# Kernel optimization log

Hardware: AMD Instinct MI355X
Metric: run time of the kernel (lower is better)

## Reference

```python
import jax, jax.numpy as jnp
import numpy as np

EPS = 1e-12  # torch F.normalize clamps the norm at 1e-12

def _l2norm(v, axis):
    n = jnp.sqrt(jnp.sum(v * v, axis=axis, keepdims=True))
    return v / jnp.maximum(n, EPS)

def setup_inputs() -> dict:
    key = jax.random.key(0)
    k1, k2, k3, k4 = jax.random.split(key, 4)
    N, C, H, W, K = 64, 64, 64, 64, 128
    alpha = 1.0
    x = jax.random.normal(k1, (N, C, H, W), dtype=jnp.float32)
    centroids = jax.random.uniform(k2, (K, C), dtype=jnp.float32)
    # conv is initialized from centroids (2*alpha*c, -alpha*||c||) but is an
    # independent parameter after init; keep the init relationship for realism.
    conv_w = 2.0 * alpha * centroids
    conv_b = -alpha * jnp.sqrt(jnp.sum(centroids * centroids, axis=1))
    return {"x": x, "centroids": centroids, "conv_w": conv_w, "conv_b": conv_b}

def reference(x, centroids, conv_w, conv_b):
    N, C, H, W = x.shape
    K = centroids.shape[0]
    # L2-normalize descriptors along channel dim
    xn = _l2norm(x, axis=1)                                   # [N,C,H,W]
    # 1x1 conv == per-pixel linear map C->K
    logits = jnp.einsum('nchw,kc->nkhw', xn, conv_w) + conv_b[None, :, None, None]
    sa = jax.nn.softmax(logits.reshape(N, K, H * W), axis=1)  # [N,K,HW]
    xf = xn.reshape(N, C, H * W)                              # [N,C,HW]
    # vlad[n,k,c] = sum_l sa[n,k,l] * (xf[n,c,l] - centroids[k,c])
    #            = (sa @ xf^T)[n,k,c] - sum_l sa[n,k,l] * centroids[k,c]
    vlad = jnp.einsum('nkl,ncl->nkc', sa, xf) - sa.sum(axis=-1)[:, :, None] * centroids[None]
    vlad = _l2norm(vlad, axis=2)            # intra-normalization per cluster
    vlad = vlad.reshape(N, K * C)
    vlad = _l2norm(vlad, axis=1)            # global L2 normalization
    return vlad
```

## Files before the change

kernel.cpp:

```cpp
#include <hip/hip_runtime.h>
#include <math.h>

#define NIMG   64
#define CDIM   64
#define HWPX   4096
#define KCL    128
#define TL     64
#define SHIFT  10.0f
#define RSQRT128 0.08838834764831845f

#define XP_S 72
#define XC_S 72
#define PH_S 72

typedef __attribute__((ext_vector_type(8))) short short8;
typedef __attribute__((ext_vector_type(4))) float f32x4;

#define MFMA(a, b, c) __builtin_amdgcn_mfma_f32_16x16x32_bf16((a), (b), (c), 0, 0, 0)

#define PERM_HI16 0x07060302u

#define BAR() do {                                          \
    asm volatile("s_waitcnt lgkmcnt(0)" ::: "memory");      \
    __builtin_amdgcn_s_barrier();                           \
    __builtin_amdgcn_sched_barrier(0);                      \
} while (0)

template <int NP>
__global__ __launch_bounds__(256, 2)
void netvlad_main(const float* __restrict__ x,
                  const float* __restrict__ conv_w,
                  const float* __restrict__ conv_b,
                  float* __restrict__ vout,
                  float* __restrict__ asout,
                  int use_atomic)
{
    constexpr int PIXPART = HWPX / NP;
    constexpr int NCHUNK  = PIXPART / TL;

    __shared__ __align__(16) short xp_hi[2][TL * XP_S], xp_lo[2][TL * XP_S];
    __shared__ __align__(16) short xc[2][CDIM * XC_S];
    __shared__ __align__(16) short ph[KCL * PH_S];
    __shared__ __align__(8) float2 redA2[2][4 * 32];
    __shared__ __align__(8) float2 sumP2[4 * 32];

    const int t   = threadIdx.x;
    const int w   = t >> 6;
    const int l   = t & 63;
    const int l15 = l & 15, l4 = l >> 4;
    const int n    = blockIdx.x / NP;
    const int part = blockIdx.x - n * NP;
    const int q    = t & 31;
    const int sg   = t >> 5;
    const int p0   = (q & 15) + ((q & 16) << 1);
    const int xslot = ((q >> 4) << 5) + 2 * (q & 15);

    short8 wh[2][2], wl[2][2];
    #pragma unroll
    for (int kt = 0; kt < 2; ++kt) {
        const int krow = (2 * w + kt) * 16 + l15;
        #pragma unroll
        for (int ks = 0; ks < 2; ++ks) {
            const float4* wp = (const float4*)(conv_w + krow * CDIM + ks * 32 + l4 * 8);
            float4 wa = wp[0], wb = wp[1];
            float wv[8] = {wa.x, wa.y, wa.z, wa.w, wb.x, wb.y, wb.z, wb.w};
            #pragma unroll
            for (int j = 0; j < 8; ++j) {
                unsigned u = __builtin_bit_cast(unsigned, wv[j]);
                wh[kt][ks][j] = (short)(u >> 16);
                float hf = __builtin_bit_cast(float, u & 0xffff0000u);
                wl[kt][ks][j] = (short)(__builtin_bit_cast(unsigned, wv[j] - hf) >> 16);
            }
        }
    }
    float cbr[2][4];
    #pragma unroll
    for (int kt = 0; kt < 2; ++kt)
        #pragma unroll
        for (int i = 0; i < 4; ++i)
            cbr[kt][i] = conv_b[(2 * w + kt) * 16 + l4 * 4 + i] - SHIFT;

    f32x4 acc2[2][4];
    #pragma unroll
    for (int a = 0; a < 2; ++a)
        #pragma unroll
        for (int b = 0; b < 4; ++b) acc2[a][b] = (f32x4)0.0f;
    float asr[2][4];
    #pragma unroll
    for (int a = 0; a < 2; ++a)
        #pragma unroll
        for (int i = 0; i < 4; ++i) asr[a][i] = 0.f;

    const float* xbase = x + (size_t)n * CDIM * HWPX + part * PIXPART;

    float xv0[8], xv1[8];

    #define LOADX(OFF) do {                                                 \
        _Pragma("unroll")                                                   \
        for (int j = 0; j < 8; ++j) {                                       \
            xv0[j] = xbase[(sg * 8 + j) * HWPX + (OFF) + p0];               \
            xv1[j] = xbase[(sg * 8 + j) * HWPX + (OFF) + p0 + 16];          \
        }                                                                   \
    } while (0)

    auto stage = [&](int buf) {
        float ssq0 = 0.f, ssq1 = 0.f;
        #pragma unroll
        for (int j = 0; j < 8; ++j) {
            ssq0 += xv0[j] * xv0[j];
            ssq1 += xv1[j] * xv1[j];
        }
        ssq0 += __shfl_xor(ssq0, 32);
        ssq1 += __shfl_xor(ssq1, 32);
        if (l < 32) redA2[buf][w * 32 + q] = make_float2(ssq0, ssq1);

        {
            unsigned uh[4], ul[4];
            #pragma unroll
            for (int jp = 0; jp < 4; ++jp) {
                const unsigned u0 = __builtin_bit_cast(unsigned, xv0[2 * jp]);
                const unsigned u1 = __builtin_bit_cast(unsigned, xv0[2 * jp + 1]);
                uh[jp] = __builtin_amdgcn_perm(u1, u0, PERM_HI16);
                const float h0 = __builtin_bit_cast(float, u0 & 0xffff0000u);
                const float h1 = __builtin_bit_cast(float, u1 & 0xffff0000u);
                const unsigned lo0 = __builtin_bit_cast(unsigned, xv0[2 * jp] - h0);
                const unsigned lo1 = __builtin_bit_cast(unsigned, xv0[2 * jp + 1] - h1);
                ul[jp] = __builtin_amdgcn_perm(lo1, lo0, PERM_HI16);
            }
            *(uint4*)&xp_hi[buf][p0 * XP_S + sg * 8] = make_uint4(uh[0], uh[1], uh[2], uh[3]);
            *(uint4*)&xp_lo[buf][p0 * XP_S + sg * 8] = make_uint4(ul[0], ul[1], ul[2], ul[3]);
        }
        {
            unsigned uh[4], ul[4];
            #pragma unroll
            for (int jp = 0; jp < 4; ++jp) {
                const unsigned u0 = __builtin_bit_cast(unsigned, xv1[2 * jp]);
                const unsigned u1 = __builtin_bit_cast(unsigned, xv1[2 * jp + 1]);
                uh[jp] = __builtin_amdgcn_perm(u1, u0, PERM_HI16);
                const float h0 = __builtin_bit_cast(float, u0 & 0xffff0000u);
                const float h1 = __builtin_bit_cast(float, u1 & 0xffff0000u);
                const unsigned lo0 = __builtin_bit_cast(unsigned, xv1[2 * jp] - h0);
                const unsigned lo1 = __builtin_bit_cast(unsigned, xv1[2 * jp + 1] - h1);
                ul[jp] = __builtin_amdgcn_perm(lo1, lo0, PERM_HI16);
            }
            *(uint4*)&xp_hi[buf][(p0 + 16) * XP_S + sg * 8] = make_uint4(uh[0], uh[1], uh[2], uh[3]);
            *(uint4*)&xp_lo[buf][(p0 + 16) * XP_S + sg * 8] = make_uint4(ul[0], ul[1], ul[2], ul[3]);
        }

        #pragma unroll
        for (int j = 0; j < 8; ++j) {
            unsigned pk;
            asm("v_cvt_pk_bf16_f32 %0, %1, %2"
                : "=v"(pk) : "v"(xv0[j]), "v"(xv1[j]));
            *(unsigned*)&xc[buf][(sg * 8 + j) * XC_S + xslot] = pk;
        }
    };

    LOADX(0);
    stage(0);
    if (NCHUNK > 1) LOADX(TL);
    BAR();

    for (int ch = 0; ch < NCHUNK; ++ch) {
        const int cur = ch & 1;

        if (ch + 1 < NCHUNK) {
            stage(cur ^ 1);
            if (ch + 2 < NCHUNK) LOADX((ch + 2) * TL);
        }

        f32x4 a1[2][4];
        #pragma unroll
        for (int a = 0; a < 2; ++a)
            #pragma unroll
            for (int b = 0; b < 4; ++b) a1[a][b] = (f32x4)0.0f;
        #pragma unroll
        for (int ks = 0; ks < 2; ++ks) {
            #pragma unroll
            for (int pt = 0; pt < 4; ++pt) {
                short8 bh = *(short8*)&xp_hi[cur][(pt * 16 + l15) * XP_S + ks * 32 + l4 * 8];
                short8 bl = *(short8*)&xp_lo[cur][(pt * 16 + l15) * XP_S + ks * 32 + l4 * 8];
                #pragma unroll
                for (int kt = 0; kt < 2; ++kt) {
                    a1[kt][pt] = MFMA(wh[kt][ks], bh, a1[kt][pt]);
                    a1[kt][pt] = MFMA(wh[kt][ks], bl, a1[kt][pt]);
                    a1[kt][pt] = MFMA(wl[kt][ks], bh, a1[kt][pt]);
                }
            }
        }

        float2 ra0 = redA2[cur][l15],           ra1 = redA2[cur][32 + l15];
        float2 ra2 = redA2[cur][64 + l15],      ra3 = redA2[cur][96 + l15];
        float2 rb0 = redA2[cur][16 + l15],      rb1 = redA2[cur][48 + l15];
        float2 rb2 = redA2[cur][80 + l15],      rb3 = redA2[cur][112 + l15];
        float rn[4];
        rn[0] = 1.0f / fmaxf(sqrtf((ra0.x + ra1.x) + (ra2.x + ra3.x)), 1e-12f);
        rn[1] = 1.0f / fmaxf(sqrtf((ra0.y + ra1.y) + (ra2.y + ra3.y)), 1e-12f);
        rn[2] = 1.0f / fmaxf(sqrtf((rb0.x + rb1.x) + (rb2.x + rb3.x)), 1e-12f);
        rn[3] = 1.0f / fmaxf(sqrtf((rb0.y + rb1.y) + (rb2.y + rb3.y)), 1e-12f);

        float e[2][4][4], sp[4] = {0.f, 0.f, 0.f, 0.f};
        #pragma unroll
        for (int kt = 0; kt < 2; ++kt)
            #pragma unroll
            for (int pt = 0; pt < 4; ++pt)
                #pragma unroll
                for (int i = 0; i < 4; ++i) {
                    float ev = __expf(fmaf(a1[kt][pt][i], rn[pt], cbr[kt][i]));
                    e[kt][pt][i] = ev;
                    sp[pt] += ev;
                }
        #pragma unroll
        for (int pt = 0; pt < 4; ++pt) {
            sp[pt] += __shfl_xor(sp[pt], 16);
            sp[pt] += __shfl_xor(sp[pt], 32);
        }
        if (l4 == 0)      sumP2[w * 32 + l15]      = make_float2(sp[0], sp[1]);
        else if (l4 == 1) sumP2[w * 32 + 16 + l15] = make_float2(sp[2], sp[3]);
        BAR();

        float2 q0 = sumP2[l15],       q1 = sumP2[32 + l15];
        float2 q2 = sumP2[64 + l15],  q3 = sumP2[96 + l15];
        float2 r0 = sumP2[16 + l15],  r1 = sumP2[48 + l15];
        float2 r2 = sumP2[80 + l15],  r3 = sumP2[112 + l15];
        float rden[4], rdn2[4];
        rden[0] = 1.0f / ((q0.x + q1.x) + (q2.x + q3.x));
        rden[1] = 1.0f / ((q0.y + q1.y) + (q2.y + q3.y));
        rden[2] = 1.0f / ((r0.x + r1.x) + (r2.x + r3.x));
        rden[3] = 1.0f / ((r0.y + r1.y) + (r2.y + r3.y));
        #pragma unroll
        for (int pt = 0; pt < 4; ++pt) rdn2[pt] = rden[pt] * rn[pt];

        #pragma unroll
        for (int kt = 0; kt < 2; ++kt)
            #pragma unroll
            for (int i = 0; i < 4; ++i) {
                const int row = (2 * w + kt) * 16 + l4 * 4 + i;
                const float e0 = e[kt][0][i], e1 = e[kt][1][i];
                const float e2 = e[kt][2][i], e3 = e[kt][3][i];
                asr[kt][i] = fmaf(e0, rden[0], asr[kt][i]);
                asr[kt][i] = fmaf(e1, rden[1], asr[kt][i]);
                asr[kt][i] = fmaf(e2, rden[2], asr[kt][i]);
                asr[kt][i] = fmaf(e3, rden[3], asr[kt][i]);
                const float p0f = e0 * rdn2[0], p1f = e1 * rdn2[1];
                const float p2f = e2 * rdn2[2], p3f = e3 * rdn2[3];
                unsigned pk01, pk23;
                asm("v_cvt_pk_bf16_f32 %0, %1, %2" : "=v"(pk01) : "v"(p0f), "v"(p1f));
                asm("v_cvt_pk_bf16_f32 %0, %1, %2" : "=v"(pk23) : "v"(p2f), "v"(p3f));
                *(unsigned*)&ph[row * PH_S + 2 * l15]      = pk01;
                *(unsigned*)&ph[row * PH_S + 32 + 2 * l15] = pk23;
            }

        {
            short8 xh2[4][2];
            #pragma unroll
            for (int ct = 0; ct < 4; ++ct)
                #pragma unroll
                for (int h = 0; h < 2; ++h)
                    xh2[ct][h] = *(short8*)&xc[cur][(ct * 16 + l15) * XC_S + h * 32 + l4 * 8];
            #pragma unroll
            for (int kt = 0; kt < 2; ++kt) {
                short8 ah0 = *(short8*)&ph[((2 * w + kt) * 16 + l15) * PH_S + l4 * 8];
                short8 ah1 = *(short8*)&ph[((2 * w + kt) * 16 + l15) * PH_S + 32 + l4 * 8];
                #pragma unroll
                for (int ct = 0; ct < 4; ++ct) {
                    acc2[kt][ct] = MFMA(ah0, xh2[ct][0], acc2[kt][ct]);
                    acc2[kt][ct] = MFMA(ah1, xh2[ct][1], acc2[kt][ct]);
                }
            }
        }
        BAR();
    }
    #undef LOADX

    float* vg = use_atomic ? vout + (size_t)n * KCL * CDIM
                           : vout + (size_t)blockIdx.x * KCL * CDIM;
    #pragma unroll
    for (int kt = 0; kt < 2; ++kt)
        #pragma unroll
        for (int ct = 0; ct < 4; ++ct)
            #pragma unroll
            for (int i = 0; i < 4; ++i) {
                const int row = (2 * w + kt) * 16 + l4 * 4 + i;
                const int col = ct * 16 + l15;
                if (use_atomic) atomicAdd(&vg[row * CDIM + col], acc2[kt][ct][i]);
                else            vg[row * CDIM + col] = acc2[kt][ct][i];
            }

    #pragma unroll
    for (int kt = 0; kt < 2; ++kt)
        #pragma unroll
        for (int i = 0; i < 4; ++i) {
            float v = asr[kt][i];
            v += __shfl_xor(v, 1); v += __shfl_xor(v, 2);
            v += __shfl_xor(v, 4); v += __shfl_xor(v, 8);
            if (l15 == 0) {
                const int row = (2 * w + kt) * 16 + l4 * 4 + i;
                if (use_atomic) atomicAdd(&asout[n * KCL + row], v);
                else            asout[blockIdx.x * KCL + row] = v;
            }
        }
}

template <int NPARTS>
__global__ __launch_bounds__(256)
void netvlad_finalize(const float* __restrict__ vpart,
                      const float* __restrict__ aspart,
                      const float* __restrict__ cent,
                      float* __restrict__ out)
{
    const int t = threadIdx.x;
    const int n  = blockIdx.x >> 3;
    const int kg = blockIdx.x & 7;
    const int k  = kg * 16 + (t >> 4);
    const int c0 = (t & 15) * 4;

    float vsum[4] = {0.f, 0.f, 0.f, 0.f};
    float av = 0.f;
    #pragma unroll
    for (int pt = 0; pt < NPARTS; ++pt) {
        const float* vg = vpart + (((size_t)n * NPARTS + pt) * KCL + k) * CDIM + c0;
        float4 a = *(const float4*)vg;
        vsum[0] += a.x; vsum[1] += a.y; vsum[2] += a.z; vsum[3] += a.w;
        av += aspart[(n * NPARTS + pt) * KCL + k];
    }

    float4 cq = *(const float4*)(cent + k * CDIM + c0);
    float cc[4] = {cq.x, cq.y, cq.z, cq.w};
    float ss = 0.f;
    #pragma unroll
    for (int j = 0; j < 4; ++j) {
        vsum[j] -= av * cc[j];
        ss += vsum[j] * vsum[j];
    }
    ss += __shfl_xor(ss, 1); ss += __shfl_xor(ss, 2);
    ss += __shfl_xor(ss, 4); ss += __shfl_xor(ss, 8);
    const float s = (1.0f / fmaxf(sqrtf(ss), 1e-12f)) * RSQRT128;

    float4 o;
    o.x = vsum[0] * s; o.y = vsum[1] * s; o.z = vsum[2] * s; o.w = vsum[3] * s;
    *(float4*)(out + (size_t)n * KCL * CDIM + k * CDIM + c0) = o;
}

extern "C" void kernel_launch(void* const* d_in, const int* in_sizes, int n_in,
                              void* d_out, int out_size, void* d_ws, size_t ws_size,
                              hipStream_t stream) {
    const float* x     = (const float*)d_in[0];
    const float* cent  = (const float*)d_in[1];
    const float* convw = (const float*)d_in[2];
    const float* convb = (const float*)d_in[3];
    float* out = (float*)d_out;

    const size_t need8 = (size_t)NIMG * 8 * (KCL * CDIM + KCL) * sizeof(float);

    if (ws_size >= need8) {
        float* vws  = (float*)d_ws;
        float* asws = vws + (size_t)NIMG * 8 * KCL * CDIM;
        netvlad_main<8><<<dim3(NIMG * 8), dim3(256), 0, stream>>>(
            x, convw, convb, vws, asws, 0);
        netvlad_finalize<8><<<dim3(NIMG * 8), dim3(256), 0, stream>>>(
            vws, asws, cent, out);
    } else {
        float* vws  = (float*)d_ws;
        float* asws = vws + (size_t)NIMG * KCL * CDIM;
        const size_t zb = (size_t)NIMG * (KCL * CDIM + KCL) * sizeof(float);
        hipMemsetAsync(d_ws, 0, zb, stream);
        netvlad_main<8><<<dim3(NIMG * 8), dim3(256), 0, stream>>>(
            x, convw, convb, vws, asws, 1);
        netvlad_finalize<1><<<dim3(NIMG * 8), dim3(256), 0, stream>>>(
            vws, asws, cent, out);
    }
}
```

Before: 122.1 us.

## Split waves 2x2 over clusters and pixels to cut cross-wave softmax reduction

Reassigns the four waves from each owning 32 clusters across all 64 pixels to a 2x2 split: each wave owns 64 clusters and 32 pixels of a chunk. The softmax denominator now needs only one partner wave's partial sum instead of four, and each wave loads fewer pixel B-fragments while reusing more weight fragments per load. In exchange, register use for weights, accumulators and softmax values doubles, which is a concern under launch_bounds(256,2). The two pixel halves' VLAD accumulators also need an extra LDS reduction and barrier at the end, and half the waves sit idle during the output writes.

Result: slower. 126.9 us (+3.9%).

```diff
diff --git a/kernel.cpp b/kernel.cpp
--- a/kernel.cpp
+++ b/kernel.cpp
@@ -42,12 +42,14 @@
     __shared__ __align__(16) short xc[2][CDIM * XC_S];
     __shared__ __align__(16) short ph[KCL * PH_S];
     __shared__ __align__(8) float2 redA2[2][4 * 32];
-    __shared__ __align__(8) float2 sumP2[4 * 32];
+    __shared__ __align__(8) float2 sumP2[4 * 16];
 
     const int t   = threadIdx.x;
     const int w   = t >> 6;
     const int l   = t & 63;
     const int l15 = l & 15, l4 = l >> 4;
+    const int kh  = w & 1;
+    const int h   = w >> 1;
     const int n    = blockIdx.x / NP;
     const int part = blockIdx.x - n * NP;
     const int q    = t & 31;
@@ -55,10 +57,10 @@
     const int p0   = (q & 15) + ((q & 16) << 1);
     const int xslot = ((q >> 4) << 5) + 2 * (q & 15);
 
-    short8 wh[2][2], wl[2][2];
-    #pragma unroll
-    for (int kt = 0; kt < 2; ++kt) {
-        const int krow = (2 * w + kt) * 16 + l15;
+    short8 wh[4][2], wl[4][2];
+    #pragma unroll
+    for (int kt = 0; kt < 4; ++kt) {
+        const int krow = kh * 64 + kt * 16 + l15;
         #pragma unroll
         for (int ks = 0; ks < 2; ++ks) {
             const float4* wp = (const float4*)(conv_w + krow * CDIM + ks * 32 + l4 * 8);
@@ -73,21 +75,21 @@
             }
         }
     }
-    float cbr[2][4];
-    #pragma unroll
-    for (int kt = 0; kt < 2; ++kt)
+    float cbr[4][4];
+    #pragma unroll
+    for (int kt = 0; kt < 4; ++kt)
         #pragma unroll
         for (int i = 0; i < 4; ++i)
-            cbr[kt][i] = conv_b[(2 * w + kt) * 16 + l4 * 4 + i] - SHIFT;
-
-    f32x4 acc2[2][4];
-    #pragma unroll
-    for (int a = 0; a < 2; ++a)
+            cbr[kt][i] = conv_b[kh * 64 + kt * 16 + l4 * 4 + i] - SHIFT;
+
+    f32x4 acc2[4][4];
+    #pragma unroll
+    for (int a = 0; a < 4; ++a)
         #pragma unroll
         for (int b = 0; b < 4; ++b) acc2[a][b] = (f32x4)0.0f;
-    float asr[2][4];
-    #pragma unroll
-    for (int a = 0; a < 2; ++a)
+    float asr[4][4];
+    #pragma unroll
+    for (int a = 0; a < 4; ++a)
         #pragma unroll
         for (int i = 0; i < 4; ++i) asr[a][i] = 0.f;
 
@@ -169,19 +171,20 @@
             if (ch + 2 < NCHUNK) LOADX((ch + 2) * TL);
         }
 
-        f32x4 a1[2][4];
-        #pragma unroll
-        for (int a = 0; a < 2; ++a)
-            #pragma unroll
-            for (int b = 0; b < 4; ++b) a1[a][b] = (f32x4)0.0f;
+        f32x4 a1[4][2];
+        #pragma unroll
+        for (int a = 0; a < 4; ++a)
+            #pragma unroll
+            for (int b = 0; b < 2; ++b) a1[a][b] = (f32x4)0.0f;
         #pragma unroll
         for (int ks = 0; ks < 2; ++ks) {
             #pragma unroll
-            for (int pt = 0; pt < 4; ++pt) {
-                short8 bh = *(short8*)&xp_hi[cur][(pt * 16 + l15) * XP_S + ks * 32 + l4 * 8];
-                short8 bl = *(short8*)&xp_lo[cur][(pt * 16 + l15) * XP_S + ks * 32 + l4 * 8];
+            for (int pt = 0; pt < 2; ++pt) {
+                const int prow = h * 32 + pt * 16 + l15;
+                short8 bh = *(short8*)&xp_hi[cur][prow * XP_S + ks * 32 + l4 * 8];
+                short8 bl = *(short8*)&xp_lo[cur][prow * XP_S + ks * 32 + l4 * 8];
                 #pragma unroll
-                for (int kt = 0; kt < 2; ++kt) {
+                for (int kt = 0; kt < 4; ++kt) {
                     a1[kt][pt] = MFMA(wh[kt][ks], bh, a1[kt][pt]);
                     a1[kt][pt] = MFMA(wh[kt][ks], bl, a1[kt][pt]);
                     a1[kt][pt] = MFMA(wl[kt][ks], bh, a1[kt][pt]);
@@ -189,21 +192,18 @@
             }
         }
 
-        float2 ra0 = redA2[cur][l15],           ra1 = redA2[cur][32 + l15];
-        float2 ra2 = redA2[cur][64 + l15],      ra3 = redA2[cur][96 + l15];
-        float2 rb0 = redA2[cur][16 + l15],      rb1 = redA2[cur][48 + l15];
-        float2 rb2 = redA2[cur][80 + l15],      rb3 = redA2[cur][112 + l15];
-        float rn[4];
+        const int qi = h * 16 + l15;
+        float2 ra0 = redA2[cur][qi],      ra1 = redA2[cur][32 + qi];
+        float2 ra2 = redA2[cur][64 + qi], ra3 = redA2[cur][96 + qi];
+        float rn[2];
         rn[0] = 1.0f / fmaxf(sqrtf((ra0.x + ra1.x) + (ra2.x + ra3.x)), 1e-12f);
         rn[1] = 1.0f / fmaxf(sqrtf((ra0.y + ra1.y) + (ra2.y + ra3.y)), 1e-12f);
-        rn[2] = 1.0f / fmaxf(sqrtf((rb0.x + rb1.x) + (rb2.x + rb3.x)), 1e-12f);
-        rn[3] = 1.0f / fmaxf(sqrtf((rb0.y + rb1.y) + (rb2.y + rb3.y)), 1e-12f);
-
-        float e[2][4][4], sp[4] = {0.f, 0.f, 0.f, 0.f};
-        #pragma unroll
-        for (int kt = 0; kt < 2; ++kt)
-            #pragma unroll
-            for (int pt = 0; pt < 4; ++pt)
+
+        float e[4][2][4], sp[2] = {0.f, 0.f};
+        #pragma unroll
+        for (int kt = 0; kt < 4; ++kt)
+            #pragma unroll
+            for (int pt = 0; pt < 2; ++pt)
                 #pragma unroll
                 for (int i = 0; i < 4; ++i) {
                     float ev = __expf(fmaf(a1[kt][pt][i], rn[pt], cbr[kt][i]));
@@ -211,95 +211,109 @@
                     sp[pt] += ev;
                 }
         #pragma unroll
-        for (int pt = 0; pt < 4; ++pt) {
+        for (int pt = 0; pt < 2; ++pt) {
             sp[pt] += __shfl_xor(sp[pt], 16);
             sp[pt] += __shfl_xor(sp[pt], 32);
         }
-        if (l4 == 0)      sumP2[w * 32 + l15]      = make_float2(sp[0], sp[1]);
-        else if (l4 == 1) sumP2[w * 32 + 16 + l15] = make_float2(sp[2], sp[3]);
+        if (l < 16) sumP2[w * 16 + l15] = make_float2(sp[0], sp[1]);
         BAR();
 
-        float2 q0 = sumP2[l15],       q1 = sumP2[32 + l15];
-        float2 q2 = sumP2[64 + l15],  q3 = sumP2[96 + l15];
-        float2 r0 = sumP2[16 + l15],  r1 = sumP2[48 + l15];
-        float2 r2 = sumP2[80 + l15],  r3 = sumP2[112 + l15];
-        float rden[4], rdn2[4];
-        rden[0] = 1.0f / ((q0.x + q1.x) + (q2.x + q3.x));
-        rden[1] = 1.0f / ((q0.y + q1.y) + (q2.y + q3.y));
-        rden[2] = 1.0f / ((r0.x + r1.x) + (r2.x + r3.x));
-        rden[3] = 1.0f / ((r0.y + r1.y) + (r2.y + r3.y));
-        #pragma unroll
-        for (int pt = 0; pt < 4; ++pt) rdn2[pt] = rden[pt] * rn[pt];
-
-        #pragma unroll
-        for (int kt = 0; kt < 2; ++kt)
+        float2 qo = sumP2[(w ^ 1) * 16 + l15];
+        float rden[2], rdn2[2];
+        rden[0] = 1.0f / (sp[0] + qo.x);
+        rden[1] = 1.0f / (sp[1] + qo.y);
+        rdn2[0] = rden[0] * rn[0];
+        rdn2[1] = rden[1] * rn[1];
+
+        #pragma unroll
+        for (int kt = 0; kt < 4; ++kt)
             #pragma unroll
             for (int i = 0; i < 4; ++i) {
-                const int row = (2 * w + kt) * 16 + l4 * 4 + i;
+                const int row = kh * 64 + kt * 16 + l4 * 4 + i;
                 const float e0 = e[kt][0][i], e1 = e[kt][1][i];
-                const float e2 = e[kt][2][i], e3 = e[kt][3][i];
                 asr[kt][i] = fmaf(e0, rden[0], asr[kt][i]);
                 asr[kt][i] = fmaf(e1, rden[1], asr[kt][i]);
-                asr[kt][i] = fmaf(e2, rden[2], asr[kt][i]);
-                asr[kt][i] = fmaf(e3, rden[3], asr[kt][i]);
-                const float p0f = e0 * rdn2[0], p1f = e1 * rdn2[1];
-                const float p2f = e2 * rdn2[2], p3f = e3 * rdn2[3];
-                unsigned pk01, pk23;
-                asm("v_cvt_pk_bf16_f32 %0, %1, %2" : "=v"(pk01) : "v"(p0f), "v"(p1f));
-                asm("v_cvt_pk_bf16_f32 %0, %1, %2" : "=v"(pk23) : "v"(p2f), "v"(p3f));
-                *(unsigned*)&ph[row * PH_S + 2 * l15]      = pk01;
-                *(unsigned*)&ph[row * PH_S + 32 + 2 * l15] = pk23;
+                const float pf0 = e0 * rdn2[0], pf1 = e1 * rdn2[1];
+                unsigned pk;
+                asm("v_cvt_pk_bf16_f32 %0, %1, %2" : "=v"(pk) : "v"(pf0), "v"(pf1));
+                *(unsigned*)&ph[row * PH_S + h * 32 + 2 * l15] = pk;
             }
 
         {
-            short8 xh2[4][2];
+            short8 xh2[4];
+            #pragma unroll
+            for (int ct = 0; ct < 4; ++ct)
+                xh2[ct] = *(short8*)&xc[cur][(ct * 16 + l15) * XC_S + h * 32 + l4 * 8];
+            #pragma unroll
+            for (int kt = 0; kt < 4; ++kt) {
+                short8 ah = *(short8*)&ph[(kh * 64 + kt * 16 + l15) * PH_S + h * 32 + l4 * 8];
+                #pragma unroll
+                for (int ct = 0; ct < 4; ++ct)
+                    acc2[kt][ct] = MFMA(ah, xh2[ct], acc2[kt][ct]);
+            }
+        }
+        BAR();
+    }
+    #undef LOADX
+
+    f32x4* vx0 = (f32x4*)&xp_hi[0][0];
+    f32x4* vx1 = (f32x4*)&xp_lo[0][0];
+    f32x4* ax  = (f32x4*)&xc[0][0];
+    f32x4* vx  = kh ? vx1 : vx0;
+    if (h == 1) {
+        #pragma unroll
+        for (int kt = 0; kt < 4; ++kt) {
+            #pragma unroll
+            for (int ct = 0; ct < 4; ++ct)
+                vx[l * 16 + kt * 4 + ct] = acc2[kt][ct];
+            f32x4 av;
+            av[0] = asr[kt][0]; av[1] = asr[kt][1];
+            av[2] = asr[kt][2]; av[3] = asr[kt][3];
+            ax[kh * 256 + l * 4 + kt] = av;
+        }
+    }
+    BAR();
+    if (h == 0) {
+        #pragma unroll
+        for (int kt = 0; kt < 4; ++kt) {
+            #pragma unroll
+            for (int ct = 0; ct < 4; ++ct) {
+                f32x4 o = vx[l * 16 + kt * 4 + ct];
+                acc2[kt][ct] += o;
+            }
+            f32x4 av = ax[kh * 256 + l * 4 + kt];
+            #pragma unroll
+            for (int i = 0; i < 4; ++i) asr[kt][i] += av[i];
+        }
+
+        float* vg = use_atomic ? vout + (size_t)n * KCL * CDIM
+                               : vout + (size_t)blockIdx.x * KCL * CDIM;
+        #pragma unroll
+        for (int kt = 0; kt < 4; ++kt)
             #pragma unroll
             for (int ct = 0; ct < 4; ++ct)
                 #pragma unroll
-                for (int h = 0; h < 2; ++h)
-                    xh2[ct][h] = *(short8*)&xc[cur][(ct * 16 + l15) * XC_S + h * 32 + l4 * 8];
-            #pragma unroll
-            for (int kt = 0; kt < 2; ++kt) {
-                short8 ah0 = *(short8*)&ph[((2 * w + kt) * 16 + l15) * PH_S + l4 * 8];
-                short8 ah1 = *(short8*)&ph[((2 * w + kt) * 16 + l15) * PH_S + 32 + l4 * 8];
-                #pragma unroll
-                for (int ct = 0; ct < 4; ++ct) {
-                    acc2[kt][ct] = MFMA(ah0, xh2[ct][0], acc2[kt][ct]);
-                    acc2[kt][ct] = MFMA(ah1, xh2[ct][1], acc2[kt][ct]);
+                for (int i = 0; i < 4; ++i) {
+                    const int row = kh * 64 + kt * 16 + l4 * 4 + i;
+                    const int col = ct * 16 + l15;
+                    if (use_atomic) atomicAdd(&vg[row * CDIM + col], acc2[kt][ct][i]);
+                    else            vg[row * CDIM + col] = acc2[kt][ct][i];
                 }
-            }
-        }
-        BAR();
-    }
-    #undef LOADX
-
-    float* vg = use_atomic ? vout + (size_t)n * KCL * CDIM
-                           : vout + (size_t)blockIdx.x * KCL * CDIM;
-    #pragma unroll
-    for (int kt = 0; kt < 2; ++kt)
-        #pragma unroll
-        for (int ct = 0; ct < 4; ++ct)
+
+        #pragma unroll
+        for (int kt = 0; kt < 4; ++kt)
             #pragma unroll
             for (int i = 0; i < 4; ++i) {
-                const int row = (2 * w + kt) * 16 + l4 * 4 + i;
-                const int col = ct * 16 + l15;
-                if (use_atomic) atomicAdd(&vg[row * CDIM + col], acc2[kt][ct][i]);
-                else            vg[row * CDIM + col] = acc2[kt][ct][i];
-            }
-
-    #pragma unroll
-    for (int kt = 0; kt < 2; ++kt)
-        #pragma unroll
-        for (int i = 0; i < 4; ++i) {
-            float v = asr[kt][i];
-            v += __shfl_xor(v, 1); v += __shfl_xor(v, 2);
-            v += __shfl_xor(v, 4); v += __shfl_xor(v, 8);
-            if (l15 == 0) {
-                const int row = (2 * w + kt) * 16 + l4 * 4 + i;
-                if (use_atomic) atomicAdd(&asout[n * KCL + row], v);
-                else            asout[blockIdx.x * KCL + row] = v;
-            }
-        }
+                float v = asr[kt][i];
+                v += __shfl_xor(v, 1); v += __shfl_xor(v, 2);
+                v += __shfl_xor(v, 4); v += __shfl_xor(v, 8);
+                if (l15 == 0) {
+                    const int row = kh * 64 + kt * 16 + l4 * 4 + i;
+                    if (use_atomic) atomicAdd(&asout[n * KCL + row], v);
+                    else            asout[blockIdx.x * KCL + row] = v;
+                }
+            }
+    }
 }
 
 template <int NPARTS>
```

## Software-pipeline softmax/first matmul of next chunk against second matmul of previous

Applied to the files above, without the earlier changes.

Splits the per-chunk body into two phases: logits MFMA plus exp, and normalisation plus VLAD MFMA. Each loop iteration now runs the VLAD phase of chunk ch-1, then staging and the logits phase of chunk ch. The partial softmax sums are double-buffered so chunk ch's sums can be written while chunk ch-1's are still needed. The intent is to overlap independent work across chunks and reduce stalls around barriers. In exchange, the exp values and norms stay live in registers across a barrier, which raises register pressure and could hurt occupancy.

Result: no change. 123.7 us (+1.3%).

```diff
diff --git a/kernel.cpp b/kernel.cpp
--- a/kernel.cpp
+++ b/kernel.cpp
@@ -42,7 +42,7 @@
     __shared__ __align__(16) short xc[2][CDIM * XC_S];
     __shared__ __align__(16) short ph[KCL * PH_S];
     __shared__ __align__(8) float2 redA2[2][4 * 32];
-    __shared__ __align__(8) float2 sumP2[4 * 32];
+    __shared__ __align__(8) float2 sumP2[2][4 * 32];
 
     const int t   = threadIdx.x;
     const int w   = t >> 6;
@@ -95,6 +95,9 @@
 
     float xv0[8], xv1[8];
 
+    float e[2][4][4];
+    float rnv[4];
+
     #define LOADX(OFF) do {                                                 \
         _Pragma("unroll")                                                   \
         for (int j = 0; j < 8; ++j) {                                       \
@@ -156,30 +159,18 @@
         }
     };
 
-    LOADX(0);
-    stage(0);
-    if (NCHUNK > 1) LOADX(TL);
-    BAR();
-
-    for (int ch = 0; ch < NCHUNK; ++ch) {
-        const int cur = ch & 1;
-
-        if (ch + 1 < NCHUNK) {
-            stage(cur ^ 1);
-            if (ch + 2 < NCHUNK) LOADX((ch + 2) * TL);
-        }
-
+    auto mm1_sec = [&](int b) {
         f32x4 a1[2][4];
         #pragma unroll
         for (int a = 0; a < 2; ++a)
             #pragma unroll
-            for (int b = 0; b < 4; ++b) a1[a][b] = (f32x4)0.0f;
+            for (int c = 0; c < 4; ++c) a1[a][c] = (f32x4)0.0f;
         #pragma unroll
         for (int ks = 0; ks < 2; ++ks) {
             #pragma unroll
             for (int pt = 0; pt < 4; ++pt) {
-                short8 bh = *(short8*)&xp_hi[cur][(pt * 16 + l15) * XP_S + ks * 32 + l4 * 8];
-                short8 bl = *(short8*)&xp_lo[cur][(pt * 16 + l15) * XP_S + ks * 32 + l4 * 8];
+                short8 bh = *(short8*)&xp_hi[b][(pt * 16 + l15) * XP_S + ks * 32 + l4 * 8];
+                short8 bl = *(short8*)&xp_lo[b][(pt * 16 + l15) * XP_S + ks * 32 + l4 * 8];
                 #pragma unroll
                 for (int kt = 0; kt < 2; ++kt) {
                     a1[kt][pt] = MFMA(wh[kt][ks], bh, a1[kt][pt]);
@@ -189,24 +180,23 @@
             }
         }
 
-        float2 ra0 = redA2[cur][l15],           ra1 = redA2[cur][32 + l15];
-        float2 ra2 = redA2[cur][64 + l15],      ra3 = redA2[cur][96 + l15];
-        float2 rb0 = redA2[cur][16 + l15],      rb1 = redA2[cur][48 + l15];
-        float2 rb2 = redA2[cur][80 + l15],      rb3 = redA2[cur][112 + l15];
-        float rn[4];
-        rn[0] = 1.0f / fmaxf(sqrtf((ra0.x + ra1.x) + (ra2.x + ra3.x)), 1e-12f);
-        rn[1] = 1.0f / fmaxf(sqrtf((ra0.y + ra1.y) + (ra2.y + ra3.y)), 1e-12f);
-        rn[2] = 1.0f / fmaxf(sqrtf((rb0.x + rb1.x) + (rb2.x + rb3.x)), 1e-12f);
-        rn[3] = 1.0f / fmaxf(sqrtf((rb0.y + rb1.y) + (rb2.y + rb3.y)), 1e-12f);
-
-        float e[2][4][4], sp[4] = {0.f, 0.f, 0.f, 0.f};
+        float2 ra0 = redA2[b][l15],           ra1 = redA2[b][32 + l15];
+        float2 ra2 = redA2[b][64 + l15],      ra3 = redA2[b][96 + l15];
+        float2 rb0 = redA2[b][16 + l15],      rb1 = redA2[b][48 + l15];
+        float2 rb2 = redA2[b][80 + l15],      rb3 = redA2[b][112 + l15];
+        rnv[0] = 1.0f / fmaxf(sqrtf((ra0.x + ra1.x) + (ra2.x + ra3.x)), 1e-12f);
+        rnv[1] = 1.0f / fmaxf(sqrtf((ra0.y + ra1.y) + (ra2.y + ra3.y)), 1e-12f);
+        rnv[2] = 1.0f / fmaxf(sqrtf((rb0.x + rb1.x) + (rb2.x + rb3.x)), 1e-12f);
+        rnv[3] = 1.0f / fmaxf(sqrtf((rb0.y + rb1.y) + (rb2.y + rb3.y)), 1e-12f);
+
+        float sp[4] = {0.f, 0.f, 0.f, 0.f};
         #pragma unroll
         for (int kt = 0; kt < 2; ++kt)
             #pragma unroll
             for (int pt = 0; pt < 4; ++pt)
                 #pragma unroll
                 for (int i = 0; i < 4; ++i) {
-                    float ev = __expf(fmaf(a1[kt][pt][i], rn[pt], cbr[kt][i]));
+                    float ev = __expf(fmaf(a1[kt][pt][i], rnv[pt], cbr[kt][i]));
                     e[kt][pt][i] = ev;
                     sp[pt] += ev;
                 }
@@ -215,21 +205,22 @@
             sp[pt] += __shfl_xor(sp[pt], 16);
             sp[pt] += __shfl_xor(sp[pt], 32);
         }
-        if (l4 == 0)      sumP2[w * 32 + l15]      = make_float2(sp[0], sp[1]);
-        else if (l4 == 1) sumP2[w * 32 + 16 + l15] = make_float2(sp[2], sp[3]);
-        BAR();
-
-        float2 q0 = sumP2[l15],       q1 = sumP2[32 + l15];
-        float2 q2 = sumP2[64 + l15],  q3 = sumP2[96 + l15];
-        float2 r0 = sumP2[16 + l15],  r1 = sumP2[48 + l15];
-        float2 r2 = sumP2[80 + l15],  r3 = sumP2[112 + l15];
+        if (l4 == 0)      sumP2[b][w * 32 + l15]      = make_float2(sp[0], sp[1]);
+        else if (l4 == 1) sumP2[b][w * 32 + 16 + l15] = make_float2(sp[2], sp[3]);
+    };
+
+    auto ph_mm2 = [&](int pb) {
+        float2 q0 = sumP2[pb][l15],       q1 = sumP2[pb][32 + l15];
+        float2 q2 = sumP2[pb][64 + l15],  q3 = sumP2[pb][96 + l15];
+        float2 r0 = sumP2[pb][16 + l15],  r1 = sumP2[pb][48 + l15];
+        float2 r2 = sumP2[pb][80 + l15],  r3 = sumP2[pb][112 + l15];
         float rden[4], rdn2[4];
         rden[0] = 1.0f / ((q0.x + q1.x) + (q2.x + q3.x));
         rden[1] = 1.0f / ((q0.y + q1.y) + (q2.y + q3.y));
         rden[2] = 1.0f / ((r0.x + r1.x) + (r2.x + r3.x));
         rden[3] = 1.0f / ((r0.y + r1.y) + (r2.y + r3.y));
         #pragma unroll
-        for (int pt = 0; pt < 4; ++pt) rdn2[pt] = rden[pt] * rn[pt];
+        for (int pt = 0; pt < 4; ++pt) rdn2[pt] = rden[pt] * rnv[pt];
 
         #pragma unroll
         for (int kt = 0; kt < 2; ++kt)
@@ -251,26 +242,42 @@
                 *(unsigned*)&ph[row * PH_S + 32 + 2 * l15] = pk23;
             }
 
-        {
-            short8 xh2[4][2];
-            #pragma unroll
-            for (int ct = 0; ct < 4; ++ct)
-                #pragma unroll
-                for (int h = 0; h < 2; ++h)
-                    xh2[ct][h] = *(short8*)&xc[cur][(ct * 16 + l15) * XC_S + h * 32 + l4 * 8];
-            #pragma unroll
-            for (int kt = 0; kt < 2; ++kt) {
-                short8 ah0 = *(short8*)&ph[((2 * w + kt) * 16 + l15) * PH_S + l4 * 8];
-                short8 ah1 = *(short8*)&ph[((2 * w + kt) * 16 + l15) * PH_S + 32 + l4 * 8];
-                #pragma unroll
-                for (int ct = 0; ct < 4; ++ct) {
-                    acc2[kt][ct] = MFMA(ah0, xh2[ct][0], acc2[kt][ct]);
-                    acc2[kt][ct] = MFMA(ah1, xh2[ct][1], acc2[kt][ct]);
-                }
-            }
-        }
+        short8 xh2[4][2];
+        #pragma unroll
+        for (int ct = 0; ct < 4; ++ct)
+            #pragma unroll
+            for (int hh = 0; hh < 2; ++hh)
+                xh2[ct][hh] = *(short8*)&xc[pb][(ct * 16 + l15) * XC_S + hh * 32 + l4 * 8];
+        #pragma unroll
+        for (int kt = 0; kt < 2; ++kt) {
+            short8 ah0 = *(short8*)&ph[((2 * w + kt) * 16 + l15) * PH_S + l4 * 8];
+            short8 ah1 = *(short8*)&ph[((2 * w + kt) * 16 + l15) * PH_S + 32 + l4 * 8];
+            #pragma unroll
+            for (int ct = 0; ct < 4; ++ct) {
+                acc2[kt][ct] = MFMA(ah0, xh2[ct][0], acc2[kt][ct]);
+                acc2[kt][ct] = MFMA(ah1, xh2[ct][1], acc2[kt][ct]);
+            }
+        }
+    };
+
+    LOADX(0);
+    stage(0);
+    if (NCHUNK > 1) LOADX(TL);
+    BAR();
+    if (NCHUNK > 1) stage(1);
+    if (NCHUNK > 2) LOADX(2 * TL);
+    mm1_sec(0);
+    BAR();
+
+    for (int ch = 1; ch < NCHUNK; ++ch) {
+        ph_mm2((ch - 1) & 1);
         BAR();
-    }
+        if (ch + 1 < NCHUNK) stage((ch + 1) & 1);
+        if (ch + 2 < NCHUNK) LOADX((ch + 2) * TL);
+        mm1_sec(ch & 1);
+        BAR();
+    }
+    ph_mm2((NCHUNK - 1) & 1);
     #undef LOADX
 
     float* vg = use_atomic ? vout + (size_t)n * KCL * CDIM
```
